# Performance work log

Hardware: AMD Instinct MI355X
Metric: run time of the kernel (lower is better)

Reference implementation:

```python
import jax, jax.numpy as jnp
import numpy as np

H = 128
IN = 13
B = 262144


def _uniform(key, shape, stdv):
    return jax.random.uniform(key, shape, jnp.float32, -stdv, stdv)


def setup_inputs() -> dict:
    key = jax.random.key(0)
    ks = jax.random.split(key, 20)
    stdv = 1.0 / np.sqrt(H)
    inp = {
        "x_in": jax.random.normal(ks[0], (B, IN), jnp.float32),
        "h_in": jax.random.normal(ks[1], (B, H), jnp.float32),
        "c_in": jax.random.normal(ks[2], (B, H), jnp.float32),
    }
    names = ["i", "f", "g", "o"]
    k = 3
    for n in names:
        inp[f"W_x{n}"] = _uniform(ks[k], (H, IN), stdv); k += 1
        inp[f"b_x{n}"] = _uniform(ks[k], (H,), stdv); k += 1
        inp[f"W_h{n}"] = _uniform(ks[k], (H, H), stdv); k += 1
        inp[f"b_h{n}"] = _uniform(ks[k], (H,), stdv); k += 1
    return inp


def hardtanh(x):
    return jnp.clip(x, -1.0, 1.0)


def reference(x_in, h_in, c_in,
              W_xi, b_xi, W_hi, b_hi,
              W_xf, b_xf, W_hf, b_hf,
              W_xg, b_xg, W_hg, b_hg,
              W_xo, b_xo, W_ho, b_ho):
    # Batch the 4 input projections and 4 hidden projections into 2 GEMMs
    Wx = jnp.concatenate([W_xi, W_xf, W_xg, W_xo], axis=0)   # [4H, IN]
    bx = jnp.concatenate([b_xi, b_xf, b_xg, b_xo], axis=0)   # [4H]
    Wh = jnp.concatenate([W_hi, W_hf, W_hg, W_ho], axis=0)   # [4H, H]
    bh = jnp.concatenate([b_hi, b_hf, b_hg, b_ho], axis=0)
    pre = x_in @ Wx.T + bx + h_in @ Wh.T + bh               # [B, 4H]
    pi, pf, pg, po = jnp.split(pre, 4, axis=1)
    i_t = jax.nn.sigmoid(pi)
    f_t = jax.nn.sigmoid(pf)
    g_t = hardtanh(pg)
    o_t = jax.nn.sigmoid(po)
    c_t = f_t * c_in + i_t * g_t
    h_t = o_t * hardtanh(c_t)
    return (h_t, h_t, c_t)
```

## Files before the change

### kernel.cpp

```cpp
#include <hip/hip_runtime.h>

#define H 128
#define INW 13
#define BATCH 262144
#define MT 64
#define LDK 168
#define KSTEPS 5
#define GRID 256
#define TPW (BATCH / MT / GRID)

typedef __attribute__((ext_vector_type(8))) short bf16x8;
typedef __attribute__((ext_vector_type(4))) float f32x4;

struct Params {
  const float* x; const float* h; const float* c;
  const float* Wx[4]; const float* bx[4];
  const float* Wh[4]; const float* bh[4];
  float* out;
};

__device__ __forceinline__ unsigned short bf16_rne(float f) {
  unsigned u = __builtin_bit_cast(unsigned, f);
  u += 0x7FFFu + ((u >> 16) & 1u);
  return (unsigned short)(u >> 16);
}
__device__ __forceinline__ float bf16_to_f(unsigned short s) {
  unsigned u = ((unsigned)s) << 16;
  return __builtin_bit_cast(float, u);
}
__device__ __forceinline__ void split2(float f, unsigned short& hi, unsigned short& lo) {
  hi = bf16_rne(f);
  lo = bf16_rne(f - bf16_to_f(hi));
}
__device__ __forceinline__ float sigf(float x) {
  return __builtin_amdgcn_rcpf(1.0f + __expf(-x));
}
__device__ __forceinline__ float clamp1(float x) {
  return fminf(fmaxf(x, -1.0f), 1.0f);
}

__global__ __launch_bounds__(512, 2) void lstm_fused(Params p) {
  __shared__ __align__(16) unsigned short lds[2][2][MT][LDK];

  const int tid  = threadIdx.x;
  const int lane = tid & 63;
  const int wave = tid >> 6;
  const int l15  = lane & 15;
  const int lq   = lane >> 4;
  const int wcol = wave * 16 + l15;
  const int koff = lq * 8;

  bf16x8 wfh[4][KSTEPS];
  bf16x8 wfl[4][KSTEPS];
  float  bias[4];
#pragma unroll
  for (int g = 0; g < 4; ++g) {
    const float* Wh = p.Wh[g];
    const float* Wx = p.Wx[g];
#pragma unroll
    for (int ks = 0; ks < KSTEPS; ++ks) {
      float w[8];
#pragma unroll
      for (int j = 0; j < 8; ++j) {
        if (ks < 4) {
          w[j] = Wh[wcol * H + ks * 32 + koff + j];
        } else {
          int kx = koff + j;
          w[j] = (kx < INW) ? Wx[wcol * INW + kx] : 0.0f;
        }
      }
      bf16x8 hi, lo;
#pragma unroll
      for (int j = 0; j < 8; ++j) {
        unsigned short a, b; split2(w[j], a, b);
        hi[j] = (short)a; lo[j] = (short)b;
      }
      wfh[g][ks] = hi; wfl[g][ks] = lo;
    }
    bias[g] = p.bx[g][wcol] + p.bh[g][wcol];
  }

  const long tile0 = (long)blockIdx.x * TPW;
  float4 hreg[4];
  float  xreg[4];

  auto issue_stage = [&](long t) {
    const long R = t * MT;
    const float4* h4 = reinterpret_cast<const float4*>(p.h);
#pragma unroll
    for (int i = 0; i < 4; ++i) {
      int idx = i * 512 + tid;
      int row = idx >> 5, c4 = idx & 31;
      hreg[i] = h4[(R + row) * (H / 4) + c4];
    }
#pragma unroll
    for (int i = 0; i < 4; ++i) {
      int idx = i * 512 + tid;
      int row = idx >> 5, cc = idx & 31;
      xreg[i] = (cc < INW) ? p.x[(R + row) * INW + cc] : 0.0f;
    }
  };

  auto write_stage = [&](int buf) {
#pragma unroll
    for (int i = 0; i < 4; ++i) {
      int idx = i * 512 + tid;
      int row = idx >> 5, c4 = idx & 31;
      unsigned short h0,h1,h2,h3,l0,l1,l2,l3;
      split2(hreg[i].x, h0, l0); split2(hreg[i].y, h1, l1);
      split2(hreg[i].z, h2, l2); split2(hreg[i].w, h3, l3);
      uint2 ph, pl;
      ph.x = (unsigned)h0 | ((unsigned)h1 << 16);
      ph.y = (unsigned)h2 | ((unsigned)h3 << 16);
      pl.x = (unsigned)l0 | ((unsigned)l1 << 16);
      pl.y = (unsigned)l2 | ((unsigned)l3 << 16);
      *reinterpret_cast<uint2*>(&lds[buf][0][row][c4 * 4]) = ph;
      *reinterpret_cast<uint2*>(&lds[buf][1][row][c4 * 4]) = pl;
    }
#pragma unroll
    for (int i = 0; i < 4; ++i) {
      int idx = i * 512 + tid;
      int row = idx >> 5, cc = idx & 31;
      unsigned short a, b; split2(xreg[i], a, b);
      lds[buf][0][row][H + cc] = a;
      lds[buf][1][row][H + cc] = b;
    }
  };

  issue_stage(tile0);
  write_stage(0);
  __syncthreads();

  float* o0 = p.out;
  float* o1 = p.out + (long)BATCH * H;
  float* o2 = p.out + 2L * (long)BATCH * H;

  for (int t = 0; t < TPW; ++t) {
    const long R  = (tile0 + t) * MT;
    const int buf = t & 1;

    float cin[4][4];
#pragma unroll
    for (int s = 0; s < 4; ++s)
#pragma unroll
      for (int q = 0; q < 4; ++q)
        cin[s][q] = p.c[(R + s * 16 + lq * 4 + q) * H + wcol];

    if (t + 1 < TPW) issue_stage(tile0 + t + 1);

#pragma unroll
    for (int s = 0; s < 4; ++s) {
      const unsigned short* ah_base = &lds[buf][0][s * 16 + l15][koff];
      const unsigned short* al_base = &lds[buf][1][s * 16 + l15][koff];
      f32x4 acc[4];
#pragma unroll
      for (int g = 0; g < 4; ++g) { f32x4 v = {bias[g], bias[g], bias[g], bias[g]}; acc[g] = v; }
#pragma unroll
      for (int ks = 0; ks < KSTEPS; ++ks) {
        bf16x8 ah = *reinterpret_cast<const bf16x8*>(ah_base + ks * 32);
        bf16x8 al = *reinterpret_cast<const bf16x8*>(al_base + ks * 32);
#pragma unroll
        for (int g = 0; g < 4; ++g) {
          acc[g] = __builtin_amdgcn_mfma_f32_16x16x32_bf16(ah, wfh[g][ks], acc[g], 0, 0, 0);
          acc[g] = __builtin_amdgcn_mfma_f32_16x16x32_bf16(al, wfh[g][ks], acc[g], 0, 0, 0);
          acc[g] = __builtin_amdgcn_mfma_f32_16x16x32_bf16(ah, wfl[g][ks], acc[g], 0, 0, 0);
        }
      }
#pragma unroll
      for (int q = 0; q < 4; ++q) {
        float it = sigf(acc[0][q]);
        float ft = sigf(acc[1][q]);
        float gt = clamp1(acc[2][q]);
        float ot = sigf(acc[3][q]);
        float ct = ft * cin[s][q] + it * gt;
        float ht = ot * clamp1(ct);
        long row = R + s * 16 + lq * 4 + q;
        o0[row * H + wcol] = ht;
        o1[row * H + wcol] = ht;
        o2[row * H + wcol] = ct;
      }
    }

    if (t + 1 < TPW) write_stage(buf ^ 1);
    __syncthreads();
  }
}

extern "C" void kernel_launch(void* const* d_in, const int* in_sizes, int n_in,
                              void* d_out, int out_size, void* d_ws, size_t ws_size,
                              hipStream_t stream) {
  (void)in_sizes; (void)n_in; (void)d_ws; (void)ws_size; (void)out_size;
  Params p;
  p.x = (const float*)d_in[0];
  p.h = (const float*)d_in[1];
  p.c = (const float*)d_in[2];
  for (int g = 0; g < 4; ++g) {
    p.Wx[g] = (const float*)d_in[3 + 4 * g];
    p.bx[g] = (const float*)d_in[4 + 4 * g];
    p.Wh[g] = (const float*)d_in[5 + 4 * g];
    p.bh[g] = (const float*)d_in[6 + 4 * g];
  }
  p.out = (float*)d_out;
  hipLaunchKernelGGL(lstm_fused, dim3(GRID), dim3(512), 0, stream, p);
}
```

Baseline: 711.4 us.

## Load A fragments directly from global into registers, drop LDS staging

Each wave now loads its own 16-row h/x fragment straight from global memory into registers in MFMA layout, with a per-step register prefetch of the next tile, instead of staging through a double-buffered LDS tile with block-wide barriers. This removes LDS traffic and __syncthreads. The cost is that every one of the 8 waves re-reads the same h rows, an 8x redundant global/L2 read of h. The bf16 split is also done 8x redundantly. Grid changes to 256 blocks of 1024 rows, each processed in 16-row steps.

```diff
diff --git a/kernel.cpp b/kernel.cpp
--- a/kernel.cpp
+++ b/kernel.cpp
@@ -3,11 +3,9 @@
 #define H 128
 #define INW 13
 #define BATCH 262144
-#define MT 64
-#define LDK 168
-#define KSTEPS 5
-#define GRID 256
-#define TPW (BATCH / MT / GRID)
+#define RPB 1024
+#define NT (RPB / 16)
+#define GRID (BATCH / RPB)
 
 typedef __attribute__((ext_vector_type(8))) short bf16x8;
 typedef __attribute__((ext_vector_type(4))) float f32x4;
@@ -28,20 +26,17 @@
   unsigned u = ((unsigned)s) << 16;
   return __builtin_bit_cast(float, u);
 }
-__device__ __forceinline__ void split2(float f, unsigned short& hi, unsigned short& lo) {
-  hi = bf16_rne(f);
-  lo = bf16_rne(f - bf16_to_f(hi));
+__device__ __forceinline__ void split2(float f, short& hi, short& lo) {
+  unsigned short h = bf16_rne(f);
+  hi = (short)h;
+  lo = (short)bf16_rne(f - bf16_to_f(h));
 }
 __device__ __forceinline__ float sigf(float x) {
   return __builtin_amdgcn_rcpf(1.0f + __expf(-x));
 }
-__device__ __forceinline__ float clamp1(float x) {
-  return fminf(fmaxf(x, -1.0f), 1.0f);
-}
+__device__ __forceinline__ float clamp1(float x) { return fminf(fmaxf(x, -1.0f), 1.0f); }
 
 __global__ __launch_bounds__(512, 2) void lstm_fused(Params p) {
-  __shared__ __align__(16) unsigned short lds[2][2][MT][LDK];
-
   const int tid  = threadIdx.x;
   const int lane = tid & 63;
   const int wave = tid >> 6;
@@ -50,139 +45,106 @@
   const int wcol = wave * 16 + l15;
   const int koff = lq * 8;
 
-  bf16x8 wfh[4][KSTEPS];
-  bf16x8 wfl[4][KSTEPS];
+  bf16x8 wfh[4][5], wfl[4][5];
   float  bias[4];
 #pragma unroll
   for (int g = 0; g < 4; ++g) {
     const float* Wh = p.Wh[g];
     const float* Wx = p.Wx[g];
 #pragma unroll
-    for (int ks = 0; ks < KSTEPS; ++ks) {
-      float w[8];
-#pragma unroll
-      for (int j = 0; j < 8; ++j) {
-        if (ks < 4) {
-          w[j] = Wh[wcol * H + ks * 32 + koff + j];
-        } else {
-          int kx = koff + j;
-          w[j] = (kx < INW) ? Wx[wcol * INW + kx] : 0.0f;
-        }
-      }
+    for (int ks = 0; ks < 5; ++ks) {
       bf16x8 hi, lo;
 #pragma unroll
       for (int j = 0; j < 8; ++j) {
-        unsigned short a, b; split2(w[j], a, b);
-        hi[j] = (short)a; lo[j] = (short)b;
+        float w;
+        if (ks < 4) {
+          w = Wh[wcol * H + ks * 32 + koff + j];
+        } else {
+          int kx = koff + j;
+          w = (kx < INW) ? Wx[wcol * INW + kx] : 0.0f;
+        }
+        short a, b; split2(w, a, b);
+        hi[j] = a; lo[j] = b;
       }
       wfh[g][ks] = hi; wfl[g][ks] = lo;
     }
     bias[g] = p.bx[g][wcol] + p.bh[g][wcol];
   }
 
-  const long tile0 = (long)blockIdx.x * TPW;
-  float4 hreg[4];
-  float  xreg[4];
-
-  auto issue_stage = [&](long t) {
-    const long R = t * MT;
-    const float4* h4 = reinterpret_cast<const float4*>(p.h);
-#pragma unroll
-    for (int i = 0; i < 4; ++i) {
-      int idx = i * 512 + tid;
-      int row = idx >> 5, c4 = idx & 31;
-      hreg[i] = h4[(R + row) * (H / 4) + c4];
-    }
-#pragma unroll
-    for (int i = 0; i < 4; ++i) {
-      int idx = i * 512 + tid;
-      int row = idx >> 5, cc = idx & 31;
-      xreg[i] = (cc < INW) ? p.x[(R + row) * INW + cc] : 0.0f;
-    }
-  };
-
-  auto write_stage = [&](int buf) {
-#pragma unroll
-    for (int i = 0; i < 4; ++i) {
-      int idx = i * 512 + tid;
-      int row = idx >> 5, c4 = idx & 31;
-      unsigned short h0,h1,h2,h3,l0,l1,l2,l3;
-      split2(hreg[i].x, h0, l0); split2(hreg[i].y, h1, l1);
-      split2(hreg[i].z, h2, l2); split2(hreg[i].w, h3, l3);
-      uint2 ph, pl;
-      ph.x = (unsigned)h0 | ((unsigned)h1 << 16);
-      ph.y = (unsigned)h2 | ((unsigned)h3 << 16);
-      pl.x = (unsigned)l0 | ((unsigned)l1 << 16);
-      pl.y = (unsigned)l2 | ((unsigned)l3 << 16);
-      *reinterpret_cast<uint2*>(&lds[buf][0][row][c4 * 4]) = ph;
-      *reinterpret_cast<uint2*>(&lds[buf][1][row][c4 * 4]) = pl;
-    }
-#pragma unroll
-    for (int i = 0; i < 4; ++i) {
-      int idx = i * 512 + tid;
-      int row = idx >> 5, cc = idx & 31;
-      unsigned short a, b; split2(xreg[i], a, b);
-      lds[buf][0][row][H + cc] = a;
-      lds[buf][1][row][H + cc] = b;
-    }
-  };
-
-  issue_stage(tile0);
-  write_stage(0);
-  __syncthreads();
-
+  const long R0 = (long)blockIdx.x * RPB;
   float* o0 = p.out;
   float* o1 = p.out + (long)BATCH * H;
   float* o2 = p.out + 2L * (long)BATCH * H;
 
-  for (int t = 0; t < TPW; ++t) {
-    const long R  = (tile0 + t) * MT;
-    const int buf = t & 1;
+  float4 rh[8];
+  float  rx[8];
+  float  cinN[4];
 
-    float cin[4][4];
+  {
+    const float4* hp = reinterpret_cast<const float4*>(p.h + (R0 + l15) * H + koff);
 #pragma unroll
-    for (int s = 0; s < 4; ++s)
+    for (int ks = 0; ks < 4; ++ks) { rh[2 * ks] = hp[ks * 8]; rh[2 * ks + 1] = hp[ks * 8 + 1]; }
+    const float* xp = p.x + (R0 + l15) * INW;
 #pragma unroll
-      for (int q = 0; q < 4; ++q)
-        cin[s][q] = p.c[(R + s * 16 + lq * 4 + q) * H + wcol];
+    for (int j = 0; j < 8; ++j) { int kx = koff + j; rx[j] = xp[kx < INW ? kx : (INW - 1)]; }
+#pragma unroll
+    for (int q = 0; q < 4; ++q) cinN[q] = p.c[(R0 + lq * 4 + q) * H + wcol];
+  }
 
-    if (t + 1 < TPW) issue_stage(tile0 + t + 1);
+  for (int t = 0; t < NT; ++t) {
+    const long arow = R0 + t * 16 + l15;
+    const long orow = R0 + t * 16 + lq * 4;
+    const bool more = (t + 1 < NT);
+    const float4* hpn = reinterpret_cast<const float4*>(p.h + (arow + 16) * H + koff);
+    const float*  xpn = p.x + (arow + 16) * INW;
+
+    float cin[4];
+#pragma unroll
+    for (int q = 0; q < 4; ++q) cin[q] = cinN[q];
+
+    f32x4 acc[4];
+#pragma unroll
+    for (int g = 0; g < 4; ++g) { f32x4 v = {bias[g], bias[g], bias[g], bias[g]}; acc[g] = v; }
 
 #pragma unroll
-    for (int s = 0; s < 4; ++s) {
-      const unsigned short* ah_base = &lds[buf][0][s * 16 + l15][koff];
-      const unsigned short* al_base = &lds[buf][1][s * 16 + l15][koff];
-      f32x4 acc[4];
+    for (int ks = 0; ks < 5; ++ks) {
+      bf16x8 ah, al;
+      if (ks < 4) {
+        float f[8];
+        f[0] = rh[2 * ks].x; f[1] = rh[2 * ks].y; f[2] = rh[2 * ks].z; f[3] = rh[2 * ks].w;
+        f[4] = rh[2 * ks + 1].x; f[5] = rh[2 * ks + 1].y; f[6] = rh[2 * ks + 1].z; f[7] = rh[2 * ks + 1].w;
 #pragma unroll
-      for (int g = 0; g < 4; ++g) { f32x4 v = {bias[g], bias[g], bias[g], bias[g]}; acc[g] = v; }
+        for (int j = 0; j < 8; ++j) { short a, b; split2(f[j], a, b); ah[j] = a; al[j] = b; }
+        if (more) { rh[2 * ks] = hpn[ks * 8]; rh[2 * ks + 1] = hpn[ks * 8 + 1]; }
+      } else {
 #pragma unroll
-      for (int ks = 0; ks < KSTEPS; ++ks) {
-        bf16x8 ah = *reinterpret_cast<const bf16x8*>(ah_base + ks * 32);
-        bf16x8 al = *reinterpret_cast<const bf16x8*>(al_base + ks * 32);
+        for (int j = 0; j < 8; ++j) { short a, b; split2(rx[j], a, b); ah[j] = a; al[j] = b; }
+        if (more) {
 #pragma unroll
-        for (int g = 0; g < 4; ++g) {
-          acc[g] = __builtin_amdgcn_mfma_f32_16x16x32_bf16(ah, wfh[g][ks], acc[g], 0, 0, 0);
-          acc[g] = __builtin_amdgcn_mfma_f32_16x16x32_bf16(al, wfh[g][ks], acc[g], 0, 0, 0);
-          acc[g] = __builtin_amdgcn_mfma_f32_16x16x32_bf16(ah, wfl[g][ks], acc[g], 0, 0, 0);
+          for (int j = 0; j < 8; ++j) { int kx = koff + j; rx[j] = xpn[kx < INW ? kx : (INW - 1)]; }
+#pragma unroll
+          for (int q = 0; q < 4; ++q) cinN[q] = p.c[(orow + 16 + q) * H + wcol];
         }
       }
 #pragma unroll
-      for (int q = 0; q < 4; ++q) {
-        float it = sigf(acc[0][q]);
-        float ft = sigf(acc[1][q]);
-        float gt = clamp1(acc[2][q]);
-        float ot = sigf(acc[3][q]);
-        float ct = ft * cin[s][q] + it * gt;
-        float ht = ot * clamp1(ct);
-        long row = R + s * 16 + lq * 4 + q;
-        o0[row * H + wcol] = ht;
-        o1[row * H + wcol] = ht;
-        o2[row * H + wcol] = ct;
+      for (int g = 0; g < 4; ++g) {
+        acc[g] = __builtin_amdgcn_mfma_f32_16x16x32_bf16(ah, wfh[g][ks], acc[g], 0, 0, 0);
+        acc[g] = __builtin_amdgcn_mfma_f32_16x16x32_bf16(al, wfh[g][ks], acc[g], 0, 0, 0);
+        acc[g] = __builtin_amdgcn_mfma_f32_16x16x32_bf16(ah, wfl[g][ks], acc[g], 0, 0, 0);
       }
     }
 
-    if (t + 1 < TPW) write_stage(buf ^ 1);
-    __syncthreads();
+#pragma unroll
+    for (int q = 0; q < 4; ++q) {
+      float it = sigf(acc[0][q]);
+      float ft = sigf(acc[1][q]);
+      float gt = clamp1(acc[2][q]);
+      float ot = sigf(acc[3][q]);
+      float ct = ft * cin[q] + it * gt;
+      float ht = ot * clamp1(ct);
+      long ro = (orow + q) * H + wcol;
+      o0[ro] = ht; o1[ro] = ht; o2[ro] = ct;
+    }
   }
 }
 
```

Measured after the change: 953.7 us. 34.1% more time.
